# Kernel optimization log

Measured on AMD Instinct MI355X. Metric: run time of the kernel, lower is better.

Reference implementation:

```python
import jax, jax.numpy as jnp
import numpy as np

H = 512
W = 512
CLAMP = 0.1


def _make_ray(K):
    # replicate torch: u, v = np.meshgrid(range(H), range(W)) -> shapes (W, H)
    u, v = np.meshgrid(np.arange(H), np.arange(W))
    uv = np.stack((u, v, np.ones_like(u)), axis=2).reshape(-1, 3).astype(np.float32)  # (W*H, 3)
    Ki = jnp.linalg.inv(K)
    return jnp.asarray(uv) @ Ki.T  # (H*W, 3)


def _grid_sample_border(img, grid):
    # img: (B, C, H, W), grid: (B, Hg, Wg, 2) in [-1, 1], bilinear, align_corners=False,
    # padding_mode='border' (torch default semantics).
    B, C, Hh, Ww = img.shape
    x = ((grid[..., 0] + 1.0) * Ww - 1.0) * 0.5
    y = ((grid[..., 1] + 1.0) * Hh - 1.0) * 0.5
    x = jnp.clip(x, 0.0, Ww - 1.0)
    y = jnp.clip(y, 0.0, Hh - 1.0)
    x0f = jnp.floor(x)
    y0f = jnp.floor(y)
    wx = (x - x0f)[:, None]  # (B,1,Hg,Wg)
    wy = (y - y0f)[:, None]
    x0 = x0f.astype(jnp.int32)
    y0 = y0f.astype(jnp.int32)
    x1 = jnp.minimum(x0 + 1, Ww - 1)
    y1 = jnp.minimum(y0 + 1, Hh - 1)

    def gather(iy, ix):
        # per-batch fancy gather: (B,C,Hg,Wg)
        return jax.vmap(lambda im, yy, xx: im[:, yy, xx])(img, iy, ix)

    v00 = gather(y0, x0)
    v01 = gather(y0, x1)
    v10 = gather(y1, x0)
    v11 = gather(y1, x1)
    return (v00 * (1 - wx) * (1 - wy) + v01 * wx * (1 - wy)
            + v10 * (1 - wx) * wy + v11 * wx * wy)


def _forward_single(depth0, depth1, R0, t0, R1, t1, rgb0, rgb1, mask0, K, ray):
    bs = depth0.shape[0]
    # unproject: xyz in world frame
    xyz = depth0.reshape(bs, -1, 1) * ray[None]           # (bs, HW, 3)
    xyz = xyz - t0[:, None, :]
    xyz = jnp.einsum('bnd,bde->bne', xyz, R0)             # bmm(xyz, R0)
    # project into camera 1
    xyz = jnp.einsum('bnd,bed->bne', xyz, R1)             # bmm(xyz, R1^T)
    xyz = xyz + t1[:, None, :]
    uv = xyz @ K.T                                        # (bs, HW, 3)
    d = uv[..., 2:3]
    uv = uv[..., :2] / (jax.nn.relu(d) + 1e-12)
    gx = uv[..., 0] / (W - 1) * 2.0 - 1.0
    gy = uv[..., 1] / (H - 1) * 2.0 - 1.0
    grid = jnp.stack([gx, gy], axis=-1).reshape(bs, H, W, 2)
    depth10 = _grid_sample_border(depth1, grid)           # (bs,1,H,W)
    rgb10 = _grid_sample_border(rgb1, grid)               # (bs,3,H,W)
    loss_d = jnp.abs(d.reshape(bs, -1) - depth10.reshape(bs, -1))
    loss_rgb = jnp.mean(jnp.abs(rgb0.reshape(bs, 3, -1) - rgb10.reshape(bs, 3, -1)), axis=1)
    m = mask0.reshape(bs, -1).astype(loss_d.dtype)
    loss_d = loss_d * m
    loss_rgb = loss_rgb * m
    if CLAMP > 0:
        mask_clamp = jax.lax.stop_gradient((loss_d < CLAMP).astype(loss_d.dtype))
        loss_d = loss_d * mask_clamp
        loss_rgb = loss_rgb * mask_clamp
    return loss_d.mean(axis=1), loss_rgb.mean(axis=1)


def setup_inputs() -> dict:
    key = jax.random.key(0)
    ks = jax.random.split(key, 12)
    bs = 16
    eye = jnp.eye(3)[None]
    K = jnp.array([[500.0, 0.0, 256.0], [0.0, 500.0, 256.0], [0.0, 0.0, 1.0]], jnp.float32)
    return {
        'depth0': jax.random.uniform(ks[0], (bs, 1, H, W)) + 0.5,
        'depth1': jax.random.uniform(ks[1], (bs, 1, H, W)) + 0.5,
        'R0': eye + 0.02 * jax.random.normal(ks[2], (bs, 3, 3)),
        't0': 0.05 * jax.random.normal(ks[3], (bs, 3)),
        'R1': eye + 0.02 * jax.random.normal(ks[4], (bs, 3, 3)),
        't1': 0.05 * jax.random.normal(ks[5], (bs, 3)),
        'rgb0': jax.random.uniform(ks[6], (bs, 3, H, W)),
        'rgb1': jax.random.uniform(ks[7], (bs, 3, H, W)),
        'mask0': jax.random.bernoulli(ks[8], 0.7, (bs, 1, H, W)),
        'mask1': jax.random.bernoulli(ks[9], 0.7, (bs, 1, H, W)),
        'K': K,
    }


def reference(depth0, depth1, R0, t0, R1, t1, rgb0, rgb1, mask0, mask1, K):
    ray = _make_ray(K)
    l0, l0_rgb = _forward_single(depth0, depth1, R0, t0, R1, t1, rgb0, rgb1, mask0, K, ray)
    l1, l1_rgb = _forward_single(depth1, depth0, R1, t1, R0, t0, rgb1, rgb0, mask1, K, ray)
    return (l0 + l1, l0_rgb + l1_rgb)
```

## Files before the change

kernel.cpp:

```cpp
#include <hip/hip_runtime.h>
#include <hip/hip_bf16.h>

#define HH 512
#define WW 512
#define NPIX (HH*WW)
#define CLAMP_V 0.1f

#define WS_XFORM 40
#define WS_PACK_OFF 4096

__device__ inline float bf16_to_f(unsigned short u) {
    union { unsigned int i; float f; } x;
    x.i = ((unsigned int)u) << 16;
    return x.f;
}
__device__ inline float lo16(unsigned int w) { return bf16_to_f((unsigned short)(w & 0xFFFFu)); }
__device__ inline float hi16(unsigned int w) { return bf16_to_f((unsigned short)(w >> 16)); }

template<bool BF16>
__device__ __forceinline__ float ldf(const void* p, int i) {
    if (BF16) return bf16_to_f(((const unsigned short*)p)[i]);
    return ((const float*)p)[i];
}
__device__ inline float ldf_rt(const void* p, int i, int bf) {
    return bf ? bf16_to_f(((const unsigned short*)p)[i]) : ((const float*)p)[i];
}

__global__ __launch_bounds__(256) void setup_kernel(
    const void* R0, const void* t0, const void* R1, const void* t1,
    const void* Kp, const void* mask0, float* ws, int capB16, int capF32)
{
    __shared__ int vio[4];
    __shared__ int sBf16;
    int tid = threadIdx.x;
    if (tid < 32) ws[tid] = 0.0f;
    if (tid == 0) {
        unsigned int k0 = ((const unsigned int*)Kp)[0];
        sBf16 = (k0 == 0x000043FAu) ? 1 : 0;
        vio[0] = vio[1] = vio[2] = vio[3] = 0;
    }
    __syncthreads();

    int v0 = 0, v1 = 0, v2 = 0, v3 = 0;
    const uint4* mi = (const uint4*)mask0;
    for (int i = tid; i < 1024; i += 256) {
        uint4 q = mi[i];
        unsigned int vv[4] = {q.x, q.y, q.z, q.w};
        #pragma unroll
        for (int j = 0; j < 4; ++j) {
            unsigned int v = vv[j];
            if (v > 1u) v0 = 1;
            if (!(v == 0u || v == 0x3F800000u)) v1 = 1;
            unsigned int lo = v & 0xFFFFu, hi = v >> 16;
            if (!((lo == 0u || lo == 0x3F80u) && (hi == 0u || hi == 0x3F80u))) v2 = 1;
            if (v & 0xFEFEFEFEu) v3 = 1;
        }
    }
    if (v0) atomicOr(&vio[0], 1);
    if (v1) atomicOr(&vio[1], 1);
    if (v2) atomicOr(&vio[2], 1);
    if (v3) atomicOr(&vio[3], 1);
    __syncthreads();
    if (tid == 0) {
        int fmt = (!vio[0]) ? 0 : ((!vio[1]) ? 1 : ((!vio[2]) ? 2 : 3));
        ((int*)ws)[32] = sBf16;
        ((int*)ws)[33] = fmt;
        ((int*)ws)[34] = sBf16 ? capB16 : capF32;
    }

    if (tid < 32) {
        int bf = sBf16;
        int dir = tid >> 4, b = tid & 15;
        float Km[9], Ki[9], Ra[9], Rb[9], ta[3], tb[3];
        for (int i = 0; i < 9; ++i) Km[i] = ldf_rt(Kp, i, bf);
        float det = Km[0]*(Km[4]*Km[8]-Km[5]*Km[7])
                  - Km[1]*(Km[3]*Km[8]-Km[5]*Km[6])
                  + Km[2]*(Km[3]*Km[7]-Km[4]*Km[6]);
        float id = 1.0f / det;
        Ki[0] = (Km[4]*Km[8]-Km[5]*Km[7])*id;
        Ki[1] = (Km[2]*Km[7]-Km[1]*Km[8])*id;
        Ki[2] = (Km[1]*Km[5]-Km[2]*Km[4])*id;
        Ki[3] = (Km[5]*Km[6]-Km[3]*Km[8])*id;
        Ki[4] = (Km[0]*Km[8]-Km[2]*Km[6])*id;
        Ki[5] = (Km[2]*Km[3]-Km[0]*Km[5])*id;
        Ki[6] = (Km[3]*Km[7]-Km[4]*Km[6])*id;
        Ki[7] = (Km[1]*Km[6]-Km[0]*Km[7])*id;
        Ki[8] = (Km[0]*Km[4]-Km[1]*Km[3])*id;

        const void* Rap = dir ? R1 : R0;
        const void* tap = dir ? t1 : t0;
        const void* Rbp = dir ? R0 : R1;
        const void* tbp = dir ? t0 : t1;
        for (int i = 0; i < 9; ++i) { Ra[i] = ldf_rt(Rap, b*9 + i, bf); Rb[i] = ldf_rt(Rbp, b*9 + i, bf); }
        for (int i = 0; i < 3; ++i) { ta[i] = ldf_rt(tap, b*3 + i, bf); tb[i] = ldf_rt(tbp, b*3 + i, bf); }

        float T[9];
        for (int i = 0; i < 3; ++i)
            for (int j = 0; j < 3; ++j)
                T[3*i+j] = Rb[3*i+0]*Ra[3*j+0] + Rb[3*i+1]*Ra[3*j+1] + Rb[3*i+2]*Ra[3*j+2];
        float M[9];
        for (int i = 0; i < 3; ++i)
            for (int j = 0; j < 3; ++j)
                M[3*i+j] = Km[3*i+0]*T[0+j] + Km[3*i+1]*T[3+j] + Km[3*i+2]*T[6+j];
        float P[9];
        for (int i = 0; i < 3; ++i)
            for (int j = 0; j < 3; ++j)
                P[3*i+j] = M[3*i+0]*Ki[0+j] + M[3*i+1]*Ki[3+j] + M[3*i+2]*Ki[6+j];
        float c[3];
        for (int i = 0; i < 3; ++i)
            c[i] = (Km[3*i+0]*tb[0] + Km[3*i+1]*tb[1] + Km[3*i+2]*tb[2])
                 - (M[3*i+0]*ta[0]  + M[3*i+1]*ta[1]  + M[3*i+2]*ta[2]);

        float* o = ws + WS_XFORM + tid*12;
        for (int i = 0; i < 9; ++i) o[i] = P[i];
        for (int i = 0; i < 3; ++i) o[9+i] = c[i];
    }
}

__global__ __launch_bounds__(256) void pack_kernel(
    const void* depth0, const void* depth1,
    const void* rgb0, const void* rgb1,
    const void* mask0, const void* mask1, float* ws)
{
    const int* wsi = (const int*)ws;
    if (wsi[34] == 0) return;
    int isBf16  = wsi[32];
    int maskFmt = wsi[33];

    unsigned int pairIdx = blockIdx.x * 256 + threadIdx.x;
    unsigned int img = pairIdx >> 21;
    unsigned int e   = pairIdx & 0x1FFFFFu;
    unsigned int b   = e >> 17;
    unsigned int p   = (e & 0x1FFFFu) * 2;
    const void* dep = img ? depth1 : depth0;
    const void* rgb = img ? rgb1   : rgb0;
    const void* msk = img ? mask1  : mask0;
    char* base = (char*)ws + WS_PACK_OFF;

    int m0, m1;
    {
        size_t e2 = (size_t)b*NPIX + p;
        if (maskFmt == 0) {
            int2 v = *(const int2*)((const int*)msk + e2);
            m0 = v.x != 0; m1 = v.y != 0;
        } else if (maskFmt == 1) {
            float2 v = *(const float2*)((const float*)msk + e2);
            m0 = v.x != 0.0f; m1 = v.y != 0.0f;
        } else if (maskFmt == 2) {
            unsigned int w = *(const unsigned int*)((const unsigned short*)msk + e2);
            m0 = (w & 0xFFFFu) != 0; m1 = (w >> 16) != 0;
        } else {
            const unsigned char* u = (const unsigned char*)msk + e2;
            m0 = u[0] != 0; m1 = u[1] != 0;
        }
    }

    if (isBf16) {
        const unsigned short* dp = (const unsigned short*)dep + b*NPIX + p;
        const unsigned short* rp = (const unsigned short*)rgb + (size_t)b*3*NPIX + p;
        unsigned int d  = *(const unsigned int*)dp;
        unsigned int r0 = *(const unsigned int*)(rp + 0*NPIX);
        unsigned int r1 = *(const unsigned int*)(rp + 1*NPIX);
        unsigned int r2 = *(const unsigned int*)(rp + 2*NPIX);
        if (!m0) d ^= 0x00008000u;
        if (!m1) d ^= 0x80000000u;
        uint4 o;
        o.x = (d  & 0xFFFFu) | (r0 << 16);
        o.y = (r1 & 0xFFFFu) | (r2 << 16);
        o.z = (d  >> 16)     | (r0 & 0xFFFF0000u);
        o.w = (r1 >> 16)     | (r2 & 0xFFFF0000u);
        ((uint4*)base)[img*(16*NPIX/2) + e] = o;
    } else {
        const float* dp = (const float*)dep + b*NPIX + p;
        const float* rp = (const float*)rgb + (size_t)b*3*NPIX + p;
        float2 d  = *(const float2*)dp;
        float2 r0 = *(const float2*)(rp + 0*NPIX);
        float2 r1 = *(const float2*)(rp + 1*NPIX);
        float2 r2 = *(const float2*)(rp + 2*NPIX);
        if (!m0) d.x = -d.x;
        if (!m1) d.y = -d.y;
        float4* ob = (float4*)base + (size_t)img*16*NPIX + b*NPIX + p;
        ob[0] = make_float4(d.x, r0.x, r1.x, r2.x);
        ob[1] = make_float4(d.y, r0.y, r1.y, r2.y);
    }
}

struct Coords {
    int i00, i01, i10, i11;
    float w00, w01, w10, w11;
    float Zc;
};

__device__ __forceinline__ Coords project(float fx, float fy, float d, const float* P)
{
    float Xc = d * (P[0]*fx + P[1]*fy + P[2]) + P[9];
    float Yc = d * (P[3]*fx + P[4]*fy + P[5]) + P[10];
    float Zc = d * (P[6]*fx + P[7]*fy + P[8]) + P[11];

    float den = fmaxf(Zc, 0.0f) + 1e-12f;
    float ux = Xc / den, uy = Yc / den;
    float gx = ux / (float)(WW-1) * 2.0f - 1.0f;
    float gy = uy / (float)(HH-1) * 2.0f - 1.0f;
    float xs = ((gx + 1.0f) * (float)WW - 1.0f) * 0.5f;
    float ys = ((gy + 1.0f) * (float)HH - 1.0f) * 0.5f;
    xs = fminf(fmaxf(xs, 0.0f), (float)(WW-1));
    ys = fminf(fmaxf(ys, 0.0f), (float)(HH-1));

    float x0f = floorf(xs), y0f = floorf(ys);
    float wx = xs - x0f, wy = ys - y0f;
    int x0 = (int)x0f, y0 = (int)y0f;
    int x1 = min(x0 + 1, WW-1), y1 = min(y0 + 1, HH-1);

    Coords C;
    C.w00 = (1.0f-wx)*(1.0f-wy); C.w01 = wx*(1.0f-wy);
    C.w10 = (1.0f-wx)*wy;        C.w11 = wx*wy;
    C.i00 = y0*WW + x0; C.i01 = y0*WW + x1;
    C.i10 = y1*WW + x0; C.i11 = y1*WW + x1;
    C.Zc = Zc;
    return C;
}

__global__ __launch_bounds__(256) void main_packed(float* ws)
{
    const int* wsi = (const int*)ws;
    if (wsi[34] == 0) return;
    int isBf16 = wsi[32];

    int xcd  = blockIdx.x & 7;
    int idx  = blockIdx.x >> 3;
    int dir  = idx >> 9;
    int b    = xcd*2 + ((idx >> 8) & 1);
    int tile = idx & 255;

    const float* Xf = ws + WS_XFORM + (dir*16 + b)*12;

    char* base = (char*)ws + WS_PACK_OFF;
    size_t imgBytes = (size_t)16*NPIX * (isBf16 ? 8 : 16);
    const char* pkSrc = base + (dir ? imgBytes : 0);
    const char* pkDst = base + (dir ? 0 : imgBytes);

    int baseB = b * NPIX;
    float sd = 0.0f, sr = 0.0f;

    #pragma unroll
    for (int k = 0; k < 4; ++k) {
        int p  = tile*1024 + k*256 + (int)threadIdx.x;
        int px = p & (WW-1), py = p >> 9;

        float d, s0, s1, s2, m;
        if (isBf16) {
            uint2 w = ((const uint2*)pkSrc)[baseB + p];
            unsigned int dbits = w.x & 0xFFFFu;
            m = (dbits & 0x8000u) ? 0.0f : 1.0f;
            d = bf16_to_f((unsigned short)(dbits & 0x7FFFu));
            s0 = hi16(w.x); s1 = lo16(w.y); s2 = hi16(w.y);
        } else {
            float4 v = ((const float4*)pkSrc)[baseB + p];
            m = (__float_as_uint(v.x) >> 31) ? 0.0f : 1.0f;
            d = fabsf(v.x);
            s0 = v.y; s1 = v.z; s2 = v.w;
        }

        if (m != 0.0f) {
            Coords A = project((float)px, (float)py, d, Xf);

            float t00d, t00r, t00g, t00b, t01d, t01r, t01g, t01b;
            float t10d, t10r, t10g, t10b, t11d, t11r, t11g, t11b;
            if (isBf16) {
                const uint2* pd = (const uint2*)pkDst + baseB;
                uint2 g00 = pd[A.i00], g01 = pd[A.i01], g10 = pd[A.i10], g11 = pd[A.i11];
                t00d = fabsf(lo16(g00.x)); t00r = hi16(g00.x); t00g = lo16(g00.y); t00b = hi16(g00.y);
                t01d = fabsf(lo16(g01.x)); t01r = hi16(g01.x); t01g = lo16(g01.y); t01b = hi16(g01.y);
                t10d = fabsf(lo16(g10.x)); t10r = hi16(g10.x); t10g = lo16(g10.y); t10b = hi16(g10.y);
                t11d = fabsf(lo16(g11.x)); t11r = hi16(g11.x); t11g = lo16(g11.y); t11b = hi16(g11.y);
            } else {
                const float4* pd = (const float4*)pkDst + baseB;
                float4 g00 = pd[A.i00], g01 = pd[A.i01], g10 = pd[A.i10], g11 = pd[A.i11];
                t00d = fabsf(g00.x); t00r = g00.y; t00g = g00.z; t00b = g00.w;
                t01d = fabsf(g01.x); t01r = g01.y; t01g = g01.z; t01b = g01.w;
                t10d = fabsf(g10.x); t10r = g10.y; t10g = g10.z; t10b = g10.w;
                t11d = fabsf(g11.x); t11r = g11.y; t11g = g11.z; t11b = g11.w;
            }

            float d10 = t00d*A.w00 + t01d*A.w01 + t10d*A.w10 + t11d*A.w11;
            float ld = fabsf(A.Zc - d10);
            float keep = (ld < CLAMP_V) ? 1.0f : 0.0f;

            float rr = t00r*A.w00 + t01r*A.w01 + t10r*A.w10 + t11r*A.w11;
            float gg = t00g*A.w00 + t01g*A.w01 + t10g*A.w10 + t11g*A.w11;
            float bb = t00b*A.w00 + t01b*A.w01 + t10b*A.w10 + t11b*A.w11;
            float ar = fabsf(s0 - rr) + fabsf(s1 - gg) + fabsf(s2 - bb);

            sd += ld * keep;
            sr += ar * (1.0f/3.0f) * keep;
        }
    }

    #pragma unroll
    for (int off = 32; off > 0; off >>= 1) {
        sd += __shfl_down(sd, off);
        sr += __shfl_down(sr, off);
    }
    __shared__ float red[8];
    int wave = threadIdx.x >> 6, lane = threadIdx.x & 63;
    if (lane == 0) { red[wave] = sd; red[4 + wave] = sr; }
    __syncthreads();
    if (threadIdx.x == 0) {
        atomicAdd(&ws[b],      red[0] + red[1] + red[2] + red[3]);
        atomicAdd(&ws[16 + b], red[4] + red[5] + red[6] + red[7]);
    }
}

template<bool BF16>
__device__ __forceinline__ void accum_dir(
    const void* dSrc, const void* dDst, const void* rSrc, const void* rDst,
    const void* msk, int maskFmt, const float* Xf, int b, int tile,
    float& sd, float& sr)
{
    int baseB = b * NPIX;
    int baseR = b * 3 * NPIX;
    #pragma unroll
    for (int k = 0; k < 4; ++k) {
        int p  = tile*1024 + k*256 + (int)threadIdx.x;
        int px = p & (WW-1), py = p >> 9;

        float d = ldf<BF16>(dSrc, baseB + p);
        Coords A = project((float)px, (float)py, d, Xf);

        float d10 = ldf<BF16>(dDst, baseB + A.i00)*A.w00
                  + ldf<BF16>(dDst, baseB + A.i01)*A.w01
                  + ldf<BF16>(dDst, baseB + A.i10)*A.w10
                  + ldf<BF16>(dDst, baseB + A.i11)*A.w11;

        float m;
        {
            int e = baseB + p;
            if      (maskFmt == 0) m = (((const int*)msk)[e]            != 0) ? 1.0f : 0.0f;
            else if (maskFmt == 1) m = (((const float*)msk)[e]          != 0.0f) ? 1.0f : 0.0f;
            else if (maskFmt == 2) m = (((const unsigned short*)msk)[e] != 0) ? 1.0f : 0.0f;
            else                   m = (((const unsigned char*)msk)[e]  != 0) ? 1.0f : 0.0f;
        }

        float ld = fabsf(A.Zc - d10) * m;
        float keep = (ld < CLAMP_V) ? 1.0f : 0.0f;
        ld *= keep;

        float ar = 0.0f;
        #pragma unroll
        for (int ch = 0; ch < 3; ++ch) {
            int cb = baseR + ch*NPIX;
            float s = ldf<BF16>(rSrc, cb + p);
            float r = ldf<BF16>(rDst, cb + A.i00)*A.w00
                    + ldf<BF16>(rDst, cb + A.i01)*A.w01
                    + ldf<BF16>(rDst, cb + A.i10)*A.w10
                    + ldf<BF16>(rDst, cb + A.i11)*A.w11;
            ar += fabsf(s - r);
        }
        sd += ld;
        sr += ar * (1.0f/3.0f) * m * keep;
    }
}

__global__ __launch_bounds__(256) void main_fallback(
    const void* depth0, const void* depth1,
    const void* rgb0, const void* rgb1,
    const void* mask0, const void* mask1, float* ws)
{
    const int* wsi = (const int*)ws;
    if (wsi[34] != 0) return;
    int isBf16  = wsi[32];
    int maskFmt = wsi[33];

    int xcd  = blockIdx.x & 7;
    int idx  = blockIdx.x >> 3;
    int b    = xcd*2 + (idx >> 8);
    int tile = idx & 255;

    const float* Xf0 = ws + WS_XFORM + (0*16 + b)*12;
    const float* Xf1 = ws + WS_XFORM + (1*16 + b)*12;

    float sd = 0.0f, sr = 0.0f;
    if (isBf16) {
        accum_dir<true >(depth0, depth1, rgb0, rgb1, mask0, maskFmt, Xf0, b, tile, sd, sr);
        accum_dir<true >(depth1, depth0, rgb1, rgb0, mask1, maskFmt, Xf1, b, tile, sd, sr);
    } else {
        accum_dir<false>(depth0, depth1, rgb0, rgb1, mask0, maskFmt, Xf0, b, tile, sd, sr);
        accum_dir<false>(depth1, depth0, rgb1, rgb0, mask1, maskFmt, Xf1, b, tile, sd, sr);
    }
    #pragma unroll
    for (int off = 32; off > 0; off >>= 1) {
        sd += __shfl_down(sd, off);
        sr += __shfl_down(sr, off);
    }
    __shared__ float red[8];
    int wave = threadIdx.x >> 6, lane = threadIdx.x & 63;
    if (lane == 0) { red[wave] = sd; red[4 + wave] = sr; }
    __syncthreads();
    if (threadIdx.x == 0) {
        atomicAdd(&ws[b],      red[0] + red[1] + red[2] + red[3]);
        atomicAdd(&ws[16 + b], red[4] + red[5] + red[6] + red[7]);
    }
}

__global__ void finalize_kernel(const float* ws, void* out)
{
    int i = threadIdx.x;
    if (i >= 32) return;
    float v = ws[i] * (1.0f / (float)NPIX);
    if (((const int*)ws)[32]) {
        ((__hip_bfloat16*)out)[i] = __float2bfloat16(v);
    } else {
        ((float*)out)[i] = v;
    }
}

extern "C" void kernel_launch(void* const* d_in, const int* in_sizes, int n_in,
                              void* d_out, int out_size, void* d_ws, size_t ws_size,
                              hipStream_t stream) {
    float* ws = (float*)d_ws;
    size_t needB16 = (size_t)WS_PACK_OFF + (size_t)2*16*NPIX*8;
    size_t needF32 = (size_t)WS_PACK_OFF + (size_t)2*16*NPIX*16;
    int capB16 = ws_size >= needB16 ? 1 : 0;
    int capF32 = ws_size >= needF32 ? 1 : 0;

    setup_kernel<<<1, 256, 0, stream>>>(d_in[2], d_in[3], d_in[4], d_in[5],
                                        d_in[10], d_in[8], ws, capB16, capF32);
    if (capB16) {
        pack_kernel<<<16384, 256, 0, stream>>>(d_in[0], d_in[1], d_in[6], d_in[7],
                                               d_in[8], d_in[9], ws);
        main_packed<<<8192, 256, 0, stream>>>(ws);
    }
    if (!capF32) {
        main_fallback<<<4096, 256, 0, stream>>>(d_in[0], d_in[1], d_in[6], d_in[7],
                                                d_in[8], d_in[9], ws);
    }
    finalize_kernel<<<1, 32, 0, stream>>>(ws, d_out);
}
```

Before: 338.0 us.

## Process both warp directions per thread in packed main kernel, halving grid

Each block now handles the same pixel tile for both directions (0→1 and 1→0) instead of one direction per block, so the grid drops from 8192 to 4096 blocks. The isBf16 branch is hoisted into a template dispatch. The two source loads and projections are issued together, which exposes more independent memory work per thread. In exchange, register pressure and per-thread work go up and there are fewer blocks, which can lower occupancy.

```diff
diff --git a/kernel.cpp b/kernel.cpp
--- a/kernel.cpp
+++ b/kernel.cpp
@@ -220,81 +220,106 @@
     return C;
 }
 
-__global__ __launch_bounds__(256) void main_packed(float* ws)
-{
-    const int* wsi = (const int*)ws;
-    if (wsi[34] == 0) return;
-    int isBf16 = wsi[32];
-
-    int xcd  = blockIdx.x & 7;
-    int idx  = blockIdx.x >> 3;
-    int dir  = idx >> 9;
-    int b    = xcd*2 + ((idx >> 8) & 1);
-    int tile = idx & 255;
-
-    const float* Xf = ws + WS_XFORM + (dir*16 + b)*12;
-
-    char* base = (char*)ws + WS_PACK_OFF;
-    size_t imgBytes = (size_t)16*NPIX * (isBf16 ? 8 : 16);
-    const char* pkSrc = base + (dir ? imgBytes : 0);
-    const char* pkDst = base + (dir ? 0 : imgBytes);
-
-    int baseB = b * NPIX;
-    float sd = 0.0f, sr = 0.0f;
-
+template<bool BF16>
+__device__ __forceinline__ void gather_accum(
+    const char* pkDst, int baseB, const Coords& A,
+    float s0, float s1, float s2, float& sd, float& sr)
+{
+    float t00d, t00r, t00g, t00b, t01d, t01r, t01g, t01b;
+    float t10d, t10r, t10g, t10b, t11d, t11r, t11g, t11b;
+    if (BF16) {
+        const uint2* pd = (const uint2*)pkDst + baseB;
+        uint2 g00 = pd[A.i00], g01 = pd[A.i01], g10 = pd[A.i10], g11 = pd[A.i11];
+        t00d = fabsf(lo16(g00.x)); t00r = hi16(g00.x); t00g = lo16(g00.y); t00b = hi16(g00.y);
+        t01d = fabsf(lo16(g01.x)); t01r = hi16(g01.x); t01g = lo16(g01.y); t01b = hi16(g01.y);
+        t10d = fabsf(lo16(g10.x)); t10r = hi16(g10.x); t10g = lo16(g10.y); t10b = hi16(g10.y);
+        t11d = fabsf(lo16(g11.x)); t11r = hi16(g11.x); t11g = lo16(g11.y); t11b = hi16(g11.y);
+    } else {
+        const float4* pd = (const float4*)pkDst + baseB;
+        float4 g00 = pd[A.i00], g01 = pd[A.i01], g10 = pd[A.i10], g11 = pd[A.i11];
+        t00d = fabsf(g00.x); t00r = g00.y; t00g = g00.z; t00b = g00.w;
+        t01d = fabsf(g01.x); t01r = g01.y; t01g = g01.z; t01b = g01.w;
+        t10d = fabsf(g10.x); t10r = g10.y; t10g = g10.z; t10b = g10.w;
+        t11d = fabsf(g11.x); t11r = g11.y; t11g = g11.z; t11b = g11.w;
+    }
+
+    float d10 = t00d*A.w00 + t01d*A.w01 + t10d*A.w10 + t11d*A.w11;
+    float ld = fabsf(A.Zc - d10);
+    float keep = (ld < CLAMP_V) ? 1.0f : 0.0f;
+
+    float rr = t00r*A.w00 + t01r*A.w01 + t10r*A.w10 + t11r*A.w11;
+    float gg = t00g*A.w00 + t01g*A.w01 + t10g*A.w10 + t11g*A.w11;
+    float bb = t00b*A.w00 + t01b*A.w01 + t10b*A.w10 + t11b*A.w11;
+    float ar = fabsf(s0 - rr) + fabsf(s1 - gg) + fabsf(s2 - bb);
+
+    sd += ld * keep;
+    sr += ar * (1.0f/3.0f) * keep;
+}
+
+template<bool BF16>
+__device__ __forceinline__ void accum_both(
+    const char* pk0, const char* pk1, const float* Xf0, const float* Xf1,
+    int baseB, int tile, float& sd, float& sr)
+{
     #pragma unroll
     for (int k = 0; k < 4; ++k) {
         int p  = tile*1024 + k*256 + (int)threadIdx.x;
         int px = p & (WW-1), py = p >> 9;
-
-        float d, s0, s1, s2, m;
-        if (isBf16) {
-            uint2 w = ((const uint2*)pkSrc)[baseB + p];
-            unsigned int dbits = w.x & 0xFFFFu;
-            m = (dbits & 0x8000u) ? 0.0f : 1.0f;
-            d = bf16_to_f((unsigned short)(dbits & 0x7FFFu));
-            s0 = hi16(w.x); s1 = lo16(w.y); s2 = hi16(w.y);
+        float fx = (float)px, fy = (float)py;
+
+        float d0, s00, s01, s02, m0;
+        float d1, s10, s11, s12, m1;
+        if (BF16) {
+            uint2 w0 = ((const uint2*)pk0)[baseB + p];
+            uint2 w1 = ((const uint2*)pk1)[baseB + p];
+            unsigned int db0 = w0.x & 0xFFFFu, db1 = w1.x & 0xFFFFu;
+            m0 = (db0 & 0x8000u) ? 0.0f : 1.0f;
+            m1 = (db1 & 0x8000u) ? 0.0f : 1.0f;
+            d0 = bf16_to_f((unsigned short)(db0 & 0x7FFFu));
+            d1 = bf16_to_f((unsigned short)(db1 & 0x7FFFu));
+            s00 = hi16(w0.x); s01 = lo16(w0.y); s02 = hi16(w0.y);
+            s10 = hi16(w1.x); s11 = lo16(w1.y); s12 = hi16(w1.y);
         } else {
-            float4 v = ((const float4*)pkSrc)[baseB + p];
-            m = (__float_as_uint(v.x) >> 31) ? 0.0f : 1.0f;
-            d = fabsf(v.x);
-            s0 = v.y; s1 = v.z; s2 = v.w;
+            float4 v0 = ((const float4*)pk0)[baseB + p];
+            float4 v1 = ((const float4*)pk1)[baseB + p];
+            m0 = (__float_as_uint(v0.x) >> 31) ? 0.0f : 1.0f;
+            m1 = (__float_as_uint(v1.x) >> 31) ? 0.0f : 1.0f;
+            d0 = fabsf(v0.x); d1 = fabsf(v1.x);
+            s00 = v0.y; s01 = v0.z; s02 = v0.w;
+            s10 = v1.y; s11 = v1.z; s12 = v1.w;
         }
 
-        if (m != 0.0f) {
-            Coords A = project((float)px, (float)py, d, Xf);
-
-            float t00d, t00r, t00g, t00b, t01d, t01r, t01g, t01b;
-            float t10d, t10r, t10g, t10b, t11d, t11r, t11g, t11b;
-            if (isBf16) {
-                const uint2* pd = (const uint2*)pkDst + baseB;
-                uint2 g00 = pd[A.i00], g01 = pd[A.i01], g10 = pd[A.i10], g11 = pd[A.i11];
-                t00d = fabsf(lo16(g00.x)); t00r = hi16(g00.x); t00g = lo16(g00.y); t00b = hi16(g00.y);
-                t01d = fabsf(lo16(g01.x)); t01r = hi16(g01.x); t01g = lo16(g01.y); t01b = hi16(g01.y);
-                t10d = fabsf(lo16(g10.x)); t10r = hi16(g10.x); t10g = lo16(g10.y); t10b = hi16(g10.y);
-                t11d = fabsf(lo16(g11.x)); t11r = hi16(g11.x); t11g = lo16(g11.y); t11b = hi16(g11.y);
-            } else {
-                const float4* pd = (const float4*)pkDst + baseB;
-                float4 g00 = pd[A.i00], g01 = pd[A.i01], g10 = pd[A.i10], g11 = pd[A.i11];
-                t00d = fabsf(g00.x); t00r = g00.y; t00g = g00.z; t00b = g00.w;
-                t01d = fabsf(g01.x); t01r = g01.y; t01g = g01.z; t01b = g01.w;
-                t10d = fabsf(g10.x); t10r = g10.y; t10g = g10.z; t10b = g10.w;
-                t11d = fabsf(g11.x); t11r = g11.y; t11g = g11.z; t11b = g11.w;
-            }
-
-            float d10 = t00d*A.w00 + t01d*A.w01 + t10d*A.w10 + t11d*A.w11;
-            float ld = fabsf(A.Zc - d10);
-            float keep = (ld < CLAMP_V) ? 1.0f : 0.0f;
-
-            float rr = t00r*A.w00 + t01r*A.w01 + t10r*A.w10 + t11r*A.w11;
-            float gg = t00g*A.w00 + t01g*A.w01 + t10g*A.w10 + t11g*A.w11;
-            float bb = t00b*A.w00 + t01b*A.w01 + t10b*A.w10 + t11b*A.w11;
-            float ar = fabsf(s0 - rr) + fabsf(s1 - gg) + fabsf(s2 - bb);
-
-            sd += ld * keep;
-            sr += ar * (1.0f/3.0f) * keep;
-        }
-    }
+        Coords A = project(fx, fy, d0, Xf0);
+        Coords B = project(fx, fy, d1, Xf1);
+
+        if (m0 != 0.0f) gather_accum<BF16>(pk1, baseB, A, s00, s01, s02, sd, sr);
+        if (m1 != 0.0f) gather_accum<BF16>(pk0, baseB, B, s10, s11, s12, sd, sr);
+    }
+}
+
+__global__ __launch_bounds__(256) void main_packed(float* ws)
+{
+    const int* wsi = (const int*)ws;
+    if (wsi[34] == 0) return;
+    int isBf16 = wsi[32];
+
+    int xcd  = blockIdx.x & 7;
+    int idx  = blockIdx.x >> 3;
+    int b    = xcd*2 + (idx >> 8);
+    int tile = idx & 255;
+
+    const float* Xf0 = ws + WS_XFORM + (0*16 + b)*12;
+    const float* Xf1 = ws + WS_XFORM + (1*16 + b)*12;
+
+    char* base = (char*)ws + WS_PACK_OFF;
+    size_t imgBytes = (size_t)16*NPIX * (isBf16 ? 8 : 16);
+    const char* pk0 = base;
+    const char* pk1 = base + imgBytes;
+
+    int baseB = b * NPIX;
+    float sd = 0.0f, sr = 0.0f;
+    if (isBf16) accum_both<true >(pk0, pk1, Xf0, Xf1, baseB, tile, sd, sr);
+    else        accum_both<false>(pk0, pk1, Xf0, Xf1, baseB, tile, sd, sr);
 
     #pragma unroll
     for (int off = 32; off > 0; off >>= 1) {
@@ -428,7 +453,7 @@
     if (capB16) {
         pack_kernel<<<16384, 256, 0, stream>>>(d_in[0], d_in[1], d_in[6], d_in[7],
                                                d_in[8], d_in[9], ws);
-        main_packed<<<8192, 256, 0, stream>>>(ws);
+        main_packed<<<4096, 256, 0, stream>>>(ws);
     }
     if (!capF32) {
         main_fallback<<<4096, 256, 0, stream>>>(d_in[0], d_in[1], d_in[6], d_in[7],
```

After: 295.1 us. 1.15x faster.
